# Kernel optimization log

Hardware: AMD Instinct MI355X
Metric: run time of the kernel (lower is better)

The kernel has to match this reference:

```python
import jax, jax.numpy as jnp
import numpy as np

N_ATOMS = 300000
N_COLS = 8
VOCAB = 4096      # nn.Embedding(4096, per_col_dim)
D_COL = 32        # per_col_dim
HID = 256         # hidden_size
N_BONDS = 320000
B_GRAPHS = 6000
ATOMS_PER_GRAPH = 50
STEPS = 3
SENTINEL = 999999999


def _linear_params(key, fan_in, fan_out):
    lim = 1.0 / np.sqrt(fan_in)
    kw, kb = jax.random.split(key)
    W = jax.random.uniform(kw, (fan_out, fan_in), minval=-lim, maxval=lim, dtype=jnp.float32)
    b = jax.random.uniform(kb, (fan_out,), minval=-lim, maxval=lim, dtype=jnp.float32)
    return W, b


def setup_inputs() -> dict:
    key = jax.random.key(0)
    ks = jax.random.split(key, 8)
    a_features = jax.random.randint(ks[0], (N_ATOMS, N_COLS), 0, VOCAB, dtype=jnp.int32)
    uv = jax.random.randint(ks[1], (N_BONDS, 2), 0, N_ATOMS, dtype=jnp.int32)
    bextra = jax.random.randint(ks[2], (N_BONDS, 1), 0, 16, dtype=jnp.int32)
    b_features = jnp.concatenate([uv, bextra], axis=1)
    # contiguous equal-length scopes: graph i owns atoms [i*50, i*50+50)
    starts = np.arange(B_GRAPHS, dtype=np.int32) * ATOMS_PER_GRAPH
    lengths = np.full(B_GRAPHS, ATOMS_PER_GRAPH, dtype=np.int32)
    a_scopes = jnp.asarray(np.stack([starts, lengths], axis=1))
    emb_weights = jax.random.normal(ks[3], (N_COLS, VOCAB, D_COL), dtype=jnp.float32) * 0.02
    W_in, b_in = _linear_params(ks[4], D_COL, HID)
    W_self, b_self = _linear_params(ks[5], HID, HID)
    W_neigh, b_neigh = _linear_params(ks[6], HID, HID)
    W_out, b_out = _linear_params(ks[7], HID, HID)
    return {
        'a_features': a_features, 'b_features': b_features, 'a_scopes': a_scopes,
        'emb_weights': emb_weights,
        'W_in': W_in, 'b_in': b_in,
        'W_self': W_self, 'b_self': b_self,
        'W_neigh': W_neigh, 'b_neigh': b_neigh,
        'W_out': W_out, 'b_out': b_out,
    }


def reference(a_features, b_features, a_scopes, emb_weights,
              W_in, b_in, W_self, b_self, W_neigh, b_neigh, W_out, b_out):
    # --- per-column embedding lookup, summed over columns ---
    idx = jnp.remainder(a_features, VOCAB)
    idx = jnp.where(a_features >= SENTINEL, 0, idx)          # sentinel -> index 0
    x = jnp.zeros((a_features.shape[0], D_COL), dtype=emb_weights.dtype)
    for c in range(N_COLS):                                   # fixed small loop over columns
        x = x + emb_weights[c][idx[:, c]]
    h = x @ W_in.T + b_in                                     # [N, HID]
    # --- undirected edges -> two directed edge lists ---
    u = b_features[:, 0]
    v = b_features[:, 1]
    src = jnp.concatenate([u, v], axis=0)
    dst = jnp.concatenate([v, u], axis=0)
    # --- message passing steps ---
    for _ in range(STEPS):
        agg = jnp.zeros_like(h).at[dst].add(h[src])           # scatter-add neighbor sum
        h = jax.nn.relu(h @ W_self.T + b_self + agg @ W_neigh.T + b_neigh)
    h = h @ W_out.T + b_out
    # --- per-graph mean pooling over contiguous scopes ---
    lengths = a_scopes[:, 1]
    seg_ids = jnp.repeat(jnp.arange(a_scopes.shape[0]), lengths,
                         total_repeat_length=h.shape[0])
    sums = jax.ops.segment_sum(h, seg_ids, num_segments=a_scopes.shape[0])
    denom = jnp.maximum(lengths, 1).astype(h.dtype)[:, None]
    return sums / denom
```

## Files before the change

### kernel.cpp

```cpp
#include <hip/hip_runtime.h>

#define NATOMS 300000
#define NCOLS 8
#define VOCABSZ 4096
#define DCOL 32
#define HIDDIM 256
#define NBONDS 320000
#define NGRAPHS 6000
#define NSTEPS 3

constexpr int MP = 300032;
constexpr int MTILES64 = MP / 64;
constexpr int HSTR = 2 * HIDDIM;
constexpr int XSTR = 2 * DCOL;

typedef _Float16 f16;
typedef _Float16 f16x8 __attribute__((ext_vector_type(8)));
typedef float f32x4 __attribute__((ext_vector_type(4)));

constexpr float LO_SCALE = 2048.0f;
constexpr float INV_LO   = 1.0f / 2048.0f;

__device__ __forceinline__ void split2(float x, f16& h, f16& l) {
    h = (f16)x;
    l = (f16)((x - (float)h) * LO_SCALE);
}

__device__ __forceinline__ int swz(int row, int q) {
    return (row * 4 + (q ^ ((row >> 1) & 3))) * 8;
}

__device__ __forceinline__ void dma16(const f16* g, f16* l) {
    __builtin_amdgcn_global_load_lds(
        (const __attribute__((address_space(1))) uint32_t*)g,
        (__attribute__((address_space(3))) uint32_t*)l, 16, 0, 0);
}

static void* g_pool = nullptr;
__attribute__((constructor)) static void alloc_pool() {
    void* p = nullptr;
    if (hipMalloc(&p, (size_t)1024 * 1024 * 1024) == hipSuccess) {
        hipMemset(p, 0, (size_t)1024 * 1024 * 1024);
        g_pool = p;
    }
}

__global__ void fill_kernel(float* out, float v, int n) {
    int i = blockIdx.x * blockDim.x + threadIdx.x;
    if (i < n) out[i] = v;
}

__global__ void build_edges_kernel(const int* __restrict__ bf, int* __restrict__ esrc,
                                   int* __restrict__ nxt, int* head) {
    int e = blockIdx.x * blockDim.x + threadIdx.x;
    if (e >= 2 * NBONDS) return;
    int src, dst;
    if (e < NBONDS) { src = bf[e * 3 + 0]; dst = bf[e * 3 + 1]; }
    else { int i = e - NBONDS; src = bf[i * 3 + 1]; dst = bf[i * 3 + 0]; }
    esrc[e] = src;
    nxt[e] = atomicExch(&head[dst], e);
}

__global__ void wsplit_kernel(const float* __restrict__ W, f16* __restrict__ Wh,
                              f16* __restrict__ Wl, int n) {
    int i = blockIdx.x * blockDim.x + threadIdx.x;
    if (i >= n) return;
    split2(W[i], Wh[i], Wl[i]);
}

__global__ void bsum_kernel(const float* __restrict__ a, const float* __restrict__ b,
                            float* __restrict__ o) {
    int i = threadIdx.x;
    o[i] = a[i] + b[i];
}

__global__ void embed_kernel(const int* __restrict__ af, const float* __restrict__ emb,
                             f16* __restrict__ x) {
    int gid = blockIdx.x * blockDim.x + threadIdx.x;
    int i = gid >> 5, k = gid & 31;
    if (i >= NATOMS) return;
    float s = 0.0f;
#pragma unroll
    for (int c = 0; c < NCOLS; c++) {
        int v = af[i * NCOLS + c];
        int idx = v & (VOCABSZ - 1);
        if (v >= 999999999) idx = 0;
        s += emb[((size_t)c * VOCABSZ + idx) * DCOL + k];
    }
    f16 hi, lo;
    split2(s, hi, lo);
    x[(size_t)i * XSTR + k] = hi;
    x[(size_t)i * XSTR + DCOL + k] = lo;
}

__global__ void agg_kernel(const f16* __restrict__ H, f16* __restrict__ G,
                           const int* __restrict__ head, const int* __restrict__ nxt,
                           const int* __restrict__ esrc) {
    int wid = (blockIdx.x * blockDim.x + threadIdx.x) >> 6;
    int lane = threadIdx.x & 63;
    if (wid >= NATOMS) return;
    float a0 = 0.f, a1 = 0.f, a2 = 0.f, a3 = 0.f,
          a4 = 0.f, a5 = 0.f, a6 = 0.f, a7 = 0.f;
    int e = head[wid];
    while (e >= 0) {
        int src = esrc[e];
        const f16x8 v = *(const f16x8*)(H + (size_t)src * HSTR + lane * 8);
        a0 += (float)v[0]; a1 += (float)v[1]; a2 += (float)v[2]; a3 += (float)v[3];
        a4 += (float)v[4]; a5 += (float)v[5]; a6 += (float)v[6]; a7 += (float)v[7];
        e = nxt[e];
    }
    const bool isLo = lane >= 32;
    if (isLo) {
        a0 *= INV_LO; a1 *= INV_LO; a2 *= INV_LO; a3 *= INV_LO;
        a4 *= INV_LO; a5 *= INV_LO; a6 *= INV_LO; a7 *= INV_LO;
    }
    float s0 = a0 + __shfl_xor(a0, 32, 64);
    float s1 = a1 + __shfl_xor(a1, 32, 64);
    float s2 = a2 + __shfl_xor(a2, 32, 64);
    float s3 = a3 + __shfl_xor(a3, 32, 64);
    float s4 = a4 + __shfl_xor(a4, 32, 64);
    float s5 = a5 + __shfl_xor(a5, 32, 64);
    float s6 = a6 + __shfl_xor(a6, 32, 64);
    float s7 = a7 + __shfl_xor(a7, 32, 64);
    f16x8 o;
#define EMIT(J, S)                                                    \
    {                                                                 \
        const f16 hv = (f16)(S);                                      \
        o[J] = isLo ? (f16)(((S) - (float)hv) * LO_SCALE) : hv;       \
    }
    EMIT(0, s0) EMIT(1, s1) EMIT(2, s2) EMIT(3, s3)
    EMIT(4, s4) EMIT(5, s5) EMIT(6, s6) EMIT(7, s7)
#undef EMIT
    *(f16x8*)(G + (size_t)wid * HSTR + lane * 8) = o;
}

template <bool HAS_A2, bool RELU, int K>
__global__ __launch_bounds__(256, 2) void mfma_gemm(
    const f16* __restrict__ A1, const f16* __restrict__ A2,
    const f16* __restrict__ B1h, const f16* __restrict__ B1l,
    const f16* __restrict__ B2h, const f16* __restrict__ B2l,
    const float* __restrict__ bias, f16* __restrict__ C) {
    constexpr int OAH = 0, OAL = 2048, OBH = 4096, OBL = 12288, BUFH = 20480;
    __shared__ __align__(16) f16 lds[2 * BUFH];

    const int t = threadIdx.x;
    const int m0 = blockIdx.x * 64;
    const int lane = t & 63;
    const int wid = t >> 6;
    const int wn = wid * 64;
    const int quad = lane >> 4;
    const int l16 = lane & 15;

    const int ra_ = wid * 16 + (lane >> 2);
    const int qs_ = (lane & 3) ^ ((ra_ >> 1) & 3);
    const int ko_ = qs_ * 8;

    f32x4 acch[4][4], accl[4][4];
#pragma unroll
    for (int a = 0; a < 4; a++)
#pragma unroll
        for (int b = 0; b < 4; b++) {
            acch[a][b] = (f32x4){0.f, 0.f, 0.f, 0.f};
            accl[a][b] = (f32x4){0.f, 0.f, 0.f, 0.f};
        }

    constexpr int NMAT = HAS_A2 ? 2 : 1;
    constexpr int NST = (K / 32) * NMAT;

#define ISSUE_STAGE(S, BUF)                                                    \
    {                                                                          \
        const int mat_ = HAS_A2 ? ((S) & 1) : 0;                               \
        const int kb_ = (HAS_A2 ? ((S) >> 1) : (S)) * 32;                      \
        const f16* A_ = (mat_ == 0) ? A1 : A2;                                 \
        const f16* Bh_ = (mat_ == 0) ? B1h : B2h;                              \
        const f16* Bl_ = (mat_ == 0) ? B1l : B2l;                              \
        f16* const dst_ = lds + (BUF) * BUFH + wid * 512;                      \
        const size_t arow_ = (size_t)(m0 + ra_) * (2 * K) + kb_ + ko_;         \
        dma16(A_ + arow_, dst_ + OAH);                                         \
        dma16(A_ + arow_ + K, dst_ + OAL);                                     \
        const size_t brow_ = (size_t)ra_ * K + kb_ + ko_;                      \
        dma16(Bh_ + brow_, dst_ + OBH);                                        \
        dma16(Bl_ + brow_, dst_ + OBL);                                        \
        dma16(Bh_ + brow_ + (size_t)64 * K, dst_ + OBH + 2048);                \
        dma16(Bl_ + brow_ + (size_t)64 * K, dst_ + OBL + 2048);                \
        dma16(Bh_ + brow_ + (size_t)128 * K, dst_ + OBH + 4096);               \
        dma16(Bl_ + brow_ + (size_t)128 * K, dst_ + OBL + 4096);               \
        dma16(Bh_ + brow_ + (size_t)192 * K, dst_ + OBH + 6144);               \
        dma16(Bl_ + brow_ + (size_t)192 * K, dst_ + OBL + 6144);               \
    }

    ISSUE_STAGE(0, 0);

    for (int s = 0; s < NST; s++) {
        asm volatile("s_waitcnt vmcnt(0)" ::: "memory");
        __syncthreads();
        if (s + 1 < NST) ISSUE_STAGE(s + 1, (s + 1) & 1);

        const f16* cb = lds + (s & 1) * BUFH;
        const f16* sAh = cb + OAH;
        const f16* sAl = cb + OAL;
        const f16* sBh = cb + OBH;
        const f16* sBl = cb + OBL;

        f16x8 fah[4], fal[4];
#pragma unroll
        for (int mt = 0; mt < 4; mt++) {
            const int src = swz(mt * 16 + l16, quad);
            fah[mt] = *(const f16x8*)(sAh + src);
            fal[mt] = *(const f16x8*)(sAl + src);
        }
#pragma unroll
        for (int nt = 0; nt < 4; nt++) {
            const int src = swz(wn + nt * 16 + l16, quad);
            const f16x8 bh = *(const f16x8*)(sBh + src);
            const f16x8 bl = *(const f16x8*)(sBl + src);
#pragma unroll
            for (int mt = 0; mt < 4; mt++) {
                acch[mt][nt] = __builtin_amdgcn_mfma_f32_16x16x32_f16(fah[mt], bh, acch[mt][nt], 0, 0, 0);
                accl[mt][nt] = __builtin_amdgcn_mfma_f32_16x16x32_f16(fah[mt], bl, accl[mt][nt], 0, 0, 0);
                accl[mt][nt] = __builtin_amdgcn_mfma_f32_16x16x32_f16(fal[mt], bh, accl[mt][nt], 0, 0, 0);
            }
        }
    }
#undef ISSUE_STAGE

#pragma unroll
    for (int mt = 0; mt < 4; mt++) {
#pragma unroll
        for (int nt = 0; nt < 4; nt++) {
            const int col = wn + nt * 16 + l16;
            const float bv = bias[col];
#pragma unroll
            for (int r = 0; r < 4; r++) {
                const int row = m0 + mt * 16 + quad * 4 + r;
                float v = acch[mt][nt][r] + accl[mt][nt][r] * INV_LO + bv;
                if (RELU) v = fmaxf(v, 0.f);
                f16 hi, lo;
                split2(v, hi, lo);
                C[(size_t)row * HSTR + col] = hi;
                C[(size_t)row * HSTR + HIDDIM + col] = lo;
            }
        }
    }
}

__global__ void readout_mean_kernel(const f16* __restrict__ H,
                                    const int* __restrict__ scopes, float* __restrict__ G) {
    int g = blockIdx.x;
    int n = threadIdx.x;
    int start = scopes[g * 2 + 0];
    int len = scopes[g * 2 + 1];
    float s = 0.f;
    for (int j = 0; j < len; j++) {
        const f16* row = H + (size_t)(start + j) * HSTR;
        s += (float)row[n] + (float)row[HIDDIM + n] * INV_LO;
    }
    int d = len > 1 ? len : 1;
    G[(size_t)g * HIDDIM + n] = s / (float)d;
}

__global__ __launch_bounds__(256) void out_gemm_kernel(
    const float* __restrict__ G, const float* __restrict__ W,
    const float* __restrict__ bias, float* __restrict__ out) {
    __shared__ float sG[16 * 256];
    const int g0 = blockIdx.x * 16;
    const int t = threadIdx.x;
#pragma unroll
    for (int i = 0; i < 16; i++) sG[i * 256 + t] = G[(size_t)(g0 + i) * 256 + t];
    __syncthreads();
    const float bv = bias[t];
    const float* wrow = W + (size_t)t * 256;
    float acc[16];
#pragma unroll
    for (int g = 0; g < 16; g++) acc[g] = 0.f;
    for (int k = 0; k < 256; k += 4) {
        const float4 w = *(const float4*)(wrow + k);
#pragma unroll
        for (int g = 0; g < 16; g++) {
            const float4 a = *(const float4*)(sG + g * 256 + k);
            acc[g] = fmaf(a.x, w.x, acc[g]);
            acc[g] = fmaf(a.y, w.y, acc[g]);
            acc[g] = fmaf(a.z, w.z, acc[g]);
            acc[g] = fmaf(a.w, w.w, acc[g]);
        }
    }
#pragma unroll
    for (int g = 0; g < 16; g++) out[(size_t)(g0 + g) * 256 + t] = acc[g] + bv;
}

extern "C" void kernel_launch(void* const* d_in, const int* in_sizes, int n_in,
                              void* d_out, int out_size, void* d_ws, size_t ws_size,
                              hipStream_t stream) {
    const int* a_features = (const int*)d_in[0];
    const int* b_features = (const int*)d_in[1];
    const int* a_scopes   = (const int*)d_in[2];
    const float* emb      = (const float*)d_in[3];
    const float* W_in     = (const float*)d_in[4];
    const float* b_in     = (const float*)d_in[5];
    const float* W_self   = (const float*)d_in[6];
    const float* b_self   = (const float*)d_in[7];
    const float* W_neigh  = (const float*)d_in[8];
    const float* b_neigh  = (const float*)d_in[9];
    const float* W_out    = (const float*)d_in[10];
    const float* b_out    = (const float*)d_in[11];

    if (g_pool == nullptr) {
        fill_kernel<<<(out_size + 255) / 256, 256, 0, stream>>>(
            (float*)d_out, 77777.0f, out_size);
        return;
    }

    f16* p = (f16*)g_pool;
    const size_t HB2 = (size_t)MP * HSTR;
    f16* bufA = p;
    f16* bufB = p + HB2;
    f16* bufC = p + 2 * HB2;
    f16* xbuf = p + 3 * HB2;
    f16* Winh = xbuf + (size_t)MP * XSTR;
    f16* Winl = Winh + HIDDIM * DCOL;
    f16* Wsh  = Winl + HIDDIM * DCOL;
    f16* Wsl  = Wsh + HIDDIM * HIDDIM;
    f16* Wnh  = Wsl + HIDDIM * HIDDIM;
    f16* Wnl  = Wnh + HIDDIM * HIDDIM;
    float* Gmean = (float*)(Wnl + HIDDIM * HIDDIM);
    float* bsum  = Gmean + (size_t)NGRAPHS * HIDDIM;
    int* esrc = (int*)(bsum + HIDDIM);
    int* nxt  = esrc + 2 * NBONDS;
    int* head = nxt + 2 * NBONDS;

    constexpr int NPAD = MP - NATOMS;

    hipMemsetAsync(head, 0xFF, (size_t)MP * sizeof(int), stream);
    build_edges_kernel<<<(2 * NBONDS + 255) / 256, 256, 0, stream>>>(b_features, esrc, nxt, head);
    wsplit_kernel<<<(HIDDIM * DCOL + 255) / 256, 256, 0, stream>>>(W_in, Winh, Winl, HIDDIM * DCOL);
    wsplit_kernel<<<(HIDDIM * HIDDIM + 255) / 256, 256, 0, stream>>>(W_self, Wsh, Wsl, HIDDIM * HIDDIM);
    wsplit_kernel<<<(HIDDIM * HIDDIM + 255) / 256, 256, 0, stream>>>(W_neigh, Wnh, Wnl, HIDDIM * HIDDIM);
    bsum_kernel<<<1, HIDDIM, 0, stream>>>(b_self, b_neigh, bsum);

    constexpr int PADH = NPAD * HSTR / 2;
    fill_kernel<<<(PADH + 255) / 256, 256, 0, stream>>>((float*)(bufA + (size_t)NATOMS * HSTR), 0.f, PADH);
    fill_kernel<<<(PADH + 255) / 256, 256, 0, stream>>>((float*)(bufB + (size_t)NATOMS * HSTR), 0.f, PADH);
    fill_kernel<<<(PADH + 255) / 256, 256, 0, stream>>>((float*)(bufC + (size_t)NATOMS * HSTR), 0.f, PADH);
    constexpr int PADX = NPAD * XSTR / 2;
    fill_kernel<<<(PADX + 255) / 256, 256, 0, stream>>>((float*)(xbuf + (size_t)NATOMS * XSTR), 0.f, PADX);

    embed_kernel<<<(NATOMS * DCOL + 255) / 256, 256, 0, stream>>>(a_features, emb, xbuf);
    mfma_gemm<false, false, DCOL><<<MTILES64, 256, 0, stream>>>(
        xbuf, nullptr, Winh, Winl, nullptr, nullptr, b_in, bufA);

    f16* h  = bufA;
    f16* g  = bufB;
    f16* hn = bufC;
    for (int s = 0; s < NSTEPS; s++) {
        agg_kernel<<<NATOMS / 4, 256, 0, stream>>>(h, g, head, nxt, esrc);
        mfma_gemm<true, true, HIDDIM><<<MTILES64, 256, 0, stream>>>(
            h, g, Wsh, Wsl, Wnh, Wnl, bsum, hn);
        f16* old = h;
        h = hn; hn = g; g = old;
    }

    readout_mean_kernel<<<NGRAPHS, 256, 0, stream>>>(h, a_scopes, Gmean);
    out_gemm_kernel<<<NGRAPHS / 16, 256, 0, stream>>>(Gmean, W_out, b_out, (float*)d_out);
}
```

Baseline: 1.936 ms.

## Pre-pack weights into MFMA fragment layout and load B directly into registers

Weights are now repacked at setup into a 16x8 fragment-major layout so each wave can read its B operands straight from global memory (L2-resident) into registers, with no LDS staging. LDS now holds only the A tile, triple-buffered with a two-stage prefetch and a finer vmcnt wait, and the MFMA issue order is regrouped by operand pair. This cuts LDS traffic and footprint, which may raise occupancy, but it puts B reads on the latency path through registers and raises register pressure.

```diff
diff --git a/kernel.cpp b/kernel.cpp
--- a/kernel.cpp
+++ b/kernel.cpp
@@ -61,11 +61,17 @@
     nxt[e] = atomicExch(&head[dst], e);
 }
 
-__global__ void wsplit_kernel(const float* __restrict__ W, f16* __restrict__ Wh,
-                              f16* __restrict__ Wl, int n) {
+__global__ void bpack_kernel(const float* __restrict__ W, f16* __restrict__ Bh,
+                             f16* __restrict__ Bl, int K, int n_total) {
     int i = blockIdx.x * blockDim.x + threadIdx.x;
-    if (i >= n) return;
-    split2(W[i], Wh[i], Wl[i]);
+    if (i >= n_total) return;
+    int n = i / K, k = i - n * K;
+    float v = W[(size_t)n * K + k];
+    int pidx = (((n >> 4) * (K >> 3) + (k >> 3)) * 16 + (n & 15)) * 8 + (k & 7);
+    f16 hi, lo;
+    split2(v, hi, lo);
+    Bh[pidx] = hi;
+    Bl[pidx] = lo;
 }
 
 __global__ void bsum_kernel(const float* __restrict__ a, const float* __restrict__ b,
@@ -140,8 +146,8 @@
     const f16* __restrict__ B1h, const f16* __restrict__ B1l,
     const f16* __restrict__ B2h, const f16* __restrict__ B2l,
     const float* __restrict__ bias, f16* __restrict__ C) {
-    constexpr int OAH = 0, OAL = 2048, OBH = 4096, OBL = 12288, BUFH = 20480;
-    __shared__ __align__(16) f16 lds[2 * BUFH];
+    constexpr int ABUF = 4096;
+    __shared__ __align__(16) f16 lds[3 * ABUF];
 
     const int t = threadIdx.x;
     const int m0 = blockIdx.x * 64;
@@ -166,42 +172,53 @@
 
     constexpr int NMAT = HAS_A2 ? 2 : 1;
     constexpr int NST = (K / 32) * NMAT;
-
-#define ISSUE_STAGE(S, BUF)                                                    \
+    constexpr int K8 = K / 8;
+
+    f16x8 rbh[4], rbhN[4], rbl[4];
+
+#define ISSUE_A(S, BI)                                                         \
     {                                                                          \
         const int mat_ = HAS_A2 ? ((S) & 1) : 0;                               \
         const int kb_ = (HAS_A2 ? ((S) >> 1) : (S)) * 32;                      \
         const f16* A_ = (mat_ == 0) ? A1 : A2;                                 \
-        const f16* Bh_ = (mat_ == 0) ? B1h : B2h;                              \
-        const f16* Bl_ = (mat_ == 0) ? B1l : B2l;                              \
-        f16* const dst_ = lds + (BUF) * BUFH + wid * 512;                      \
+        f16* const dst_ = lds + (BI) * ABUF + wid * 512;                       \
         const size_t arow_ = (size_t)(m0 + ra_) * (2 * K) + kb_ + ko_;         \
-        dma16(A_ + arow_, dst_ + OAH);                                         \
-        dma16(A_ + arow_ + K, dst_ + OAL);                                     \
-        const size_t brow_ = (size_t)ra_ * K + kb_ + ko_;                      \
-        dma16(Bh_ + brow_, dst_ + OBH);                                        \
-        dma16(Bl_ + brow_, dst_ + OBL);                                        \
-        dma16(Bh_ + brow_ + (size_t)64 * K, dst_ + OBH + 2048);                \
-        dma16(Bl_ + brow_ + (size_t)64 * K, dst_ + OBL + 2048);                \
-        dma16(Bh_ + brow_ + (size_t)128 * K, dst_ + OBH + 4096);               \
-        dma16(Bl_ + brow_ + (size_t)128 * K, dst_ + OBL + 4096);               \
-        dma16(Bh_ + brow_ + (size_t)192 * K, dst_ + OBH + 6144);               \
-        dma16(Bl_ + brow_ + (size_t)192 * K, dst_ + OBL + 6144);               \
-    }
-
-    ISSUE_STAGE(0, 0);
-
-    for (int s = 0; s < NST; s++) {
-        asm volatile("s_waitcnt vmcnt(0)" ::: "memory");
-        __syncthreads();
-        if (s + 1 < NST) ISSUE_STAGE(s + 1, (s + 1) & 1);
-
-        const f16* cb = lds + (s & 1) * BUFH;
-        const f16* sAh = cb + OAH;
-        const f16* sAl = cb + OAL;
-        const f16* sBh = cb + OBH;
-        const f16* sBl = cb + OBL;
-
+        dma16(A_ + arow_, dst_);                                               \
+        dma16(A_ + arow_ + K, dst_ + 2048);                                    \
+    }
+
+#define LOAD_B4(S, PH, DEST)                                                   \
+    {                                                                          \
+        const int mat_ = HAS_A2 ? ((S) & 1) : 0;                               \
+        const int kb8_ = (HAS_A2 ? ((S) >> 1) : (S)) * 4;                      \
+        const f16* Bp_ = (PH) ? (mat_ == 0 ? B1h : B2h)                        \
+                              : (mat_ == 0 ? B1l : B2l);                       \
+        const f16x8* pb_ =                                                     \
+            (const f16x8*)(Bp_ + ((size_t)(wn >> 4) * K8 + kb8_) * 128);       \
+        DEST[0] = pb_[lane];                                                   \
+        DEST[1] = pb_[lane + K8 * 16];                                         \
+        DEST[2] = pb_[lane + K8 * 32];                                         \
+        DEST[3] = pb_[lane + K8 * 48];                                         \
+    }
+
+    ISSUE_A(0, 0);
+    asm volatile("" ::: "memory");
+    if (NST > 1) ISSUE_A(1, 1);
+    asm volatile("" ::: "memory");
+    LOAD_B4(0, 1, rbhN);
+    asm volatile("" ::: "memory");
+
+    int bufs = 0;
+    for (int s = 0; s < NST - 1; s++) {
+        LOAD_B4(s, 0, rbl);
+        asm volatile("s_waitcnt vmcnt(10) lgkmcnt(0)" ::: "memory");
+        __builtin_amdgcn_s_barrier();
+        if (s + 2 < NST) {
+            int bI = bufs + 2; if (bI >= 3) bI -= 3;
+            ISSUE_A(s + 2, bI);
+        }
+        const f16* sAh = lds + bufs * ABUF;
+        const f16* sAl = sAh + 2048;
         f16x8 fah[4], fal[4];
 #pragma unroll
         for (int mt = 0; mt < 4; mt++) {
@@ -210,19 +227,60 @@
             fal[mt] = *(const f16x8*)(sAl + src);
         }
 #pragma unroll
-        for (int nt = 0; nt < 4; nt++) {
-            const int src = swz(wn + nt * 16 + l16, quad);
-            const f16x8 bh = *(const f16x8*)(sBh + src);
-            const f16x8 bl = *(const f16x8*)(sBl + src);
-#pragma unroll
-            for (int mt = 0; mt < 4; mt++) {
-                acch[mt][nt] = __builtin_amdgcn_mfma_f32_16x16x32_f16(fah[mt], bh, acch[mt][nt], 0, 0, 0);
-                accl[mt][nt] = __builtin_amdgcn_mfma_f32_16x16x32_f16(fah[mt], bl, accl[mt][nt], 0, 0, 0);
-                accl[mt][nt] = __builtin_amdgcn_mfma_f32_16x16x32_f16(fal[mt], bh, accl[mt][nt], 0, 0, 0);
-            }
-        }
-    }
-#undef ISSUE_STAGE
+        for (int i = 0; i < 4; i++) rbh[i] = rbhN[i];
+        LOAD_B4(s + 1, 1, rbhN);
+#pragma unroll
+        for (int nt = 0; nt < 4; nt++)
+#pragma unroll
+            for (int mt = 0; mt < 4; mt++)
+                acch[mt][nt] = __builtin_amdgcn_mfma_f32_16x16x32_f16(fah[mt], rbh[nt], acch[mt][nt], 0, 0, 0);
+#pragma unroll
+        for (int nt = 0; nt < 4; nt++)
+#pragma unroll
+            for (int mt = 0; mt < 4; mt++)
+                accl[mt][nt] = __builtin_amdgcn_mfma_f32_16x16x32_f16(fal[mt], rbh[nt], accl[mt][nt], 0, 0, 0);
+#pragma unroll
+        for (int nt = 0; nt < 4; nt++)
+#pragma unroll
+            for (int mt = 0; mt < 4; mt++)
+                accl[mt][nt] = __builtin_amdgcn_mfma_f32_16x16x32_f16(fah[mt], rbl[nt], accl[mt][nt], 0, 0, 0);
+        bufs = (bufs == 2) ? 0 : bufs + 1;
+    }
+
+    {
+        const int s = NST - 1;
+        LOAD_B4(s, 0, rbl);
+        asm volatile("s_waitcnt vmcnt(8) lgkmcnt(0)" ::: "memory");
+        __builtin_amdgcn_s_barrier();
+        const f16* sAh = lds + bufs * ABUF;
+        const f16* sAl = sAh + 2048;
+        f16x8 fah[4], fal[4];
+#pragma unroll
+        for (int mt = 0; mt < 4; mt++) {
+            const int src = swz(mt * 16 + l16, quad);
+            fah[mt] = *(const f16x8*)(sAh + src);
+            fal[mt] = *(const f16x8*)(sAl + src);
+        }
+#pragma unroll
+        for (int i = 0; i < 4; i++) rbh[i] = rbhN[i];
+#pragma unroll
+        for (int nt = 0; nt < 4; nt++)
+#pragma unroll
+            for (int mt = 0; mt < 4; mt++)
+                acch[mt][nt] = __builtin_amdgcn_mfma_f32_16x16x32_f16(fah[mt], rbh[nt], acch[mt][nt], 0, 0, 0);
+#pragma unroll
+        for (int nt = 0; nt < 4; nt++)
+#pragma unroll
+            for (int mt = 0; mt < 4; mt++)
+                accl[mt][nt] = __builtin_amdgcn_mfma_f32_16x16x32_f16(fal[mt], rbh[nt], accl[mt][nt], 0, 0, 0);
+#pragma unroll
+        for (int nt = 0; nt < 4; nt++)
+#pragma unroll
+            for (int mt = 0; mt < 4; mt++)
+                accl[mt][nt] = __builtin_amdgcn_mfma_f32_16x16x32_f16(fah[mt], rbl[nt], accl[mt][nt], 0, 0, 0);
+    }
+#undef ISSUE_A
+#undef LOAD_B4
 
 #pragma unroll
     for (int mt = 0; mt < 4; mt++) {
@@ -332,9 +390,9 @@
 
     hipMemsetAsync(head, 0xFF, (size_t)MP * sizeof(int), stream);
     build_edges_kernel<<<(2 * NBONDS + 255) / 256, 256, 0, stream>>>(b_features, esrc, nxt, head);
-    wsplit_kernel<<<(HIDDIM * DCOL + 255) / 256, 256, 0, stream>>>(W_in, Winh, Winl, HIDDIM * DCOL);
-    wsplit_kernel<<<(HIDDIM * HIDDIM + 255) / 256, 256, 0, stream>>>(W_self, Wsh, Wsl, HIDDIM * HIDDIM);
-    wsplit_kernel<<<(HIDDIM * HIDDIM + 255) / 256, 256, 0, stream>>>(W_neigh, Wnh, Wnl, HIDDIM * HIDDIM);
+    bpack_kernel<<<(HIDDIM * DCOL + 255) / 256, 256, 0, stream>>>(W_in, Winh, Winl, DCOL, HIDDIM * DCOL);
+    bpack_kernel<<<(HIDDIM * HIDDIM + 255) / 256, 256, 0, stream>>>(W_self, Wsh, Wsl, HIDDIM, HIDDIM * HIDDIM);
+    bpack_kernel<<<(HIDDIM * HIDDIM + 255) / 256, 256, 0, stream>>>(W_neigh, Wnh, Wnl, HIDDIM, HIDDIM * HIDDIM);
     bsum_kernel<<<1, HIDDIM, 0, stream>>>(b_self, b_neigh, bsum);
 
     constexpr int PADH = NPAD * HSTR / 2;
```

Result: slower. 2.043 ms (+5.5%).
